# Performance work log

Measured on AMD Instinct MI355X. Metric: run time of the kernel, lower is better.

Reference implementation:

```python
import jax, jax.numpy as jnp
import numpy as np

N_EMBD = 1024
N_HEAD = 16
HEAD_DIM = N_EMBD // N_HEAD

def setup_inputs() -> dict:
    key = jax.random.key(0)
    ks = jax.random.split(key, 9)
    B, T, C = 2, 2048, N_EMBD
    s = 1.0 / np.sqrt(C)
    x = jax.random.normal(ks[0], (B, T, C), dtype=jnp.float32)
    Wk = jax.random.normal(ks[1], (C, C), dtype=jnp.float32) * s
    bk = jnp.zeros((C,), dtype=jnp.float32)
    Wq = jax.random.normal(ks[2], (C, C), dtype=jnp.float32) * s
    bq = jnp.zeros((C,), dtype=jnp.float32)
    Wv = jax.random.normal(ks[3], (C, C), dtype=jnp.float32) * s
    bv = jnp.zeros((C,), dtype=jnp.float32)
    Wp = jax.random.normal(ks[4], (C, C), dtype=jnp.float32) * s
    bp = jnp.zeros((C,), dtype=jnp.float32)
    return {"x": x, "Wq": Wq, "bq": bq, "Wk": Wk, "bk": bk, "Wv": Wv, "bv": bv, "Wp": Wp, "bp": bp}

def reference(x, Wq, bq, Wk, bk, Wv, bv, Wp, bp):
    B, T, C = x.shape
    H, D = N_HEAD, HEAD_DIM
    # QKV projections (torch Linear: x @ W.T + b; here W is stored as (in,out))
    q = (x @ Wq + bq).reshape(B, T, H, D).transpose(0, 2, 1, 3)  # [B,H,T,D]
    k = (x @ Wk + bk).reshape(B, T, H, D).transpose(0, 2, 1, 3)
    v = (x @ Wv + bv).reshape(B, T, H, D).transpose(0, 2, 1, 3)
    att = jnp.einsum('bhtd,bhsd->bhts', q, k) / jnp.sqrt(jnp.float32(D))
    causal = jnp.tril(jnp.ones((T, T), dtype=bool))
    att = jnp.where(causal, att, jnp.float32(-jnp.inf))
    att = jax.nn.softmax(att, axis=-1)
    y = jnp.einsum('bhts,bhsd->bhtd', att, v)  # [B,H,T,D]
    y = y.transpose(0, 2, 1, 3).reshape(B, T, C)
    return y @ Wp + bp
```

## Files before the change

### kernel.cpp

```cpp
#include <hip/hip_runtime.h>
#include <cstdint>

typedef __attribute__((ext_vector_type(4))) short s16x4;
typedef __attribute__((ext_vector_type(8))) short s16x8;
typedef __attribute__((ext_vector_type(4))) float f32x4;
typedef __attribute__((ext_vector_type(16))) float f32x16;

#define L2E 1.44269504088896340736f

__device__ __forceinline__ short f2bf(float f) {
  union { float f; unsigned u; } v; v.f = f;
  unsigned r = (v.u + 0x7fffu + ((v.u >> 16) & 1u)) >> 16;
  return (short)r;
}

__device__ __forceinline__ float xhalf_f(float x) {
  union { float f; unsigned u; } a; a.f = x;
  auto r = __builtin_amdgcn_permlane32_swap(a.u, a.u, false, false);
  union { unsigned u; float f; } b;
  b.u = (threadIdx.x & 32) ? r[0] : r[1];
  return b.f;
}

typedef const __attribute__((address_space(1))) unsigned int* gas_p;
typedef __attribute__((address_space(3))) unsigned int* las_p;
__device__ __forceinline__ void stage16(const void* g, void* l) {
  __builtin_amdgcn_global_load_lds((gas_p)(uintptr_t)g,
                                   (las_p)(unsigned int)(uintptr_t)l, 16, 0, 0);
}

__global__ __launch_bounds__(256) void prepass(const float* __restrict__ W0,
                                               const float* __restrict__ W1,
                                               const float* __restrict__ W2,
                                               const float* __restrict__ W3,
                                               short* __restrict__ wdst,
                                               const float* __restrict__ x,
                                               short* __restrict__ xb) {
  const int z = blockIdx.z;
  const int t = threadIdx.x;
  if (z >= 4) {
    int i = ((z - 4) * 256 + blockIdx.y * 16 + blockIdx.x) * 256 + t;
    const f32x4* p = (const f32x4*)x + (size_t)i * 2;
    f32x4 a = p[0], b = p[1];
    s16x8 o;
    o[0] = f2bf(a[0]); o[1] = f2bf(a[1]); o[2] = f2bf(a[2]); o[3] = f2bf(a[3]);
    o[4] = f2bf(b[0]); o[5] = f2bf(b[1]); o[6] = f2bf(b[2]); o[7] = f2bf(b[3]);
    *((s16x8*)xb + i) = o;
    return;
  }
  __shared__ float tile[64][65];
  const float* in = (z == 0) ? W0 : (z == 1) ? W1 : (z == 2) ? W2 : W3;
  short* out = wdst + (size_t)z * 1048576;
  const int bi = blockIdx.y, bj = blockIdx.x;
  const int c = t & 63, r0 = t >> 6;
#pragma unroll
  for (int i = 0; i < 16; i++) {
    int r = r0 + i * 4;
    tile[r][c] = in[(size_t)(bi * 64 + r) * 1024 + bj * 64 + c];
  }
  __syncthreads();
#pragma unroll
  for (int i = 0; i < 16; i++) {
    int r = r0 + i * 4;
    out[(size_t)(bj * 64 + r) * 1024 + bi * 64 + c] = f2bf(tile[c][r]);
  }
}

template <int EPI, int BM>
__global__ __launch_bounds__(BM * 2) void gemm_bt(
    const short* __restrict__ A, const short* __restrict__ B, int N, int K,
    const float* __restrict__ b0, const float* __restrict__ b1,
    const float* __restrict__ b2, short* __restrict__ o0, short* __restrict__ o1,
    short* __restrict__ o2, float* __restrict__ ofp) {
  constexpr int T = BM * 2;
  constexpr int AR = 2;
  constexpr int BR = 512 / T;
  constexpr int BUFB = (BM + 128) * 32;
  __shared__ short L[2 * BUFB];
  const int tid = threadIdx.x;
  const int lane = tid & 63;
  const int wave = tid >> 6;
  const int wr = wave >> 1, wc = wave & 1;
  const int l15 = lane & 15, l4 = lane >> 4;
  const int id = blockIdx.x + gridDim.x * blockIdx.y;
  const int cpx = gridDim.x >> 3;
  const int xcd = id & 7, sub = id >> 3;
  const int m0 = (sub / cpx) * BM;
  const int n0 = (xcd * cpx + sub % cpx) * 128;
  f32x4 acc[4][4];
#pragma unroll
  for (int i = 0; i < 4; i++)
#pragma unroll
    for (int j = 0; j < 4; j++) acc[i][j] = (f32x4){0.f, 0.f, 0.f, 0.f};

  const int lq = tid & 3, lr = tid >> 2;
  int soffA[AR], goffA[AR];
#pragma unroll
  for (int i = 0; i < AR; i++) {
    const int r = i * (T / 4) + lr;
    soffA[i] = r * 32 + lq * 8;
    goffA[i] = r * K + lq * 8;
  }
  int soffB[BR], goffB[BR];
#pragma unroll
  for (int j = 0; j < BR; j++) {
    const int r = j * (T / 4) + lr;
    soffB[j] = BM * 32 + r * 32 + lq * 8;
    goffB[j] = r * K + lq * 8;
  }

  const short* Asrc = A + (size_t)m0 * K;
  const short* Bsrc = B + (size_t)n0 * K;
  short* bufC = L;
  short* bufN = L + BUFB;

#define GSTAGE(BUF)                                                            \
  {                                                                            \
    _Pragma("unroll") for (int i_ = 0; i_ < AR; i_++)                          \
        stage16(Asrc + goffA[i_], (BUF) + soffA[i_]);                          \
    _Pragma("unroll") for (int j_ = 0; j_ < BR; j_++)                          \
        stage16(Bsrc + goffB[j_], (BUF) + soffB[j_]);                          \
    Asrc += 32; Bsrc += 32;                                                    \
  }

  GSTAGE(bufC)
  const int NK = K >> 5;
  for (int kt = 0; kt < NK; kt++) {
    __syncthreads();
    if (kt + 1 < NK) GSTAGE(bufN)
    s16x8 af[4], bfr[4];
#pragma unroll
    for (int i = 0; i < 4; i++) {
      af[i] = *(const s16x8*)(bufC + (wr * 64 + i * 16 + l15) * 32 + l4 * 8);
      bfr[i] = *(const s16x8*)(bufC + BM * 32 + (wc * 64 + i * 16 + l15) * 32 + l4 * 8);
    }
#pragma unroll
    for (int mi = 0; mi < 4; mi++)
#pragma unroll
      for (int ni = 0; ni < 4; ni++)
        acc[mi][ni] = __builtin_amdgcn_mfma_f32_16x16x32_bf16(af[mi], bfr[ni],
                                                              acc[mi][ni], 0, 0, 0);
    short* t_ = bufC; bufC = bufN; bufN = t_;
  }
#undef GSTAGE

#pragma unroll
  for (int ni = 0; ni < 4; ni++) {
    const int col = n0 + wc * 64 + ni * 16 + l15;
    if (EPI == 1) {
      const float bias = b0[col];
#pragma unroll
      for (int mi = 0; mi < 4; mi++)
#pragma unroll
        for (int r = 0; r < 4; r++) {
          int row = m0 + wr * 64 + mi * 16 + l4 * 4 + r;
          ofp[(size_t)row * N + col] = acc[mi][ni][r] + bias;
        }
    } else {
      const float* bp; short* dst; int c1; int isV = 0; float scl = 1.0f;
      if (col < 1024) { bp = b0; dst = o0; c1 = col; scl = 0.125f * L2E; }
      else if (col < 2048) { bp = b1; dst = o1; c1 = col - 1024; }
      else { bp = b2; dst = o2; c1 = col - 2048; isV = 1; }
      const float bias = bp[c1];
      const int h = c1 >> 6, d = c1 & 63;
      if (isV) {
#pragma unroll
        for (int mi = 0; mi < 4; mi++) {
          int t0 = m0 + wr * 64 + mi * 16 + l4 * 4;
          int bb = t0 >> 11, t = t0 & 2047;
          s16x4 ov;
#pragma unroll
          for (int r = 0; r < 4; r++) ov[r] = f2bf(acc[mi][ni][r] + bias);
          *(s16x4*)(dst + (size_t)((bb * 16 + h) * 64 + d) * 2048 + t) = ov;
        }
      } else {
#pragma unroll
        for (int mi = 0; mi < 4; mi++)
#pragma unroll
          for (int r = 0; r < 4; r++) {
            int row = m0 + wr * 64 + mi * 16 + l4 * 4 + r;
            int bb = row >> 11, t = row & 2047;
            float v = (acc[mi][ni][r] + bias) * scl;
            dst[(size_t)((bb * 16 + h) * 2048 + t) * 64 + d] = f2bf(v);
          }
      }
    }
  }
}

__global__ __launch_bounds__(128) void attn_v8(const short* __restrict__ Q,
                                               const short* __restrict__ K,
                                               const short* __restrict__ Vt,
                                               short* __restrict__ Y) {
  __shared__ short Ks[2][64 * 64];
  __shared__ short Vs[3][64 * 64];
  const int bh = blockIdx.x;
  const int y = blockIdx.y;
  const int g = y >> 3, r_ = y & 7;
  const int qbase = (g << 3) | ((g & 1) ? (7 - r_) : r_);
  const int qt = (qbase + ((bh & 3) << 3)) & 31;
  const int tid = threadIdx.x, lane = tid & 63, wave = tid >> 6;
  const int q31 = lane & 31, hi = lane >> 5;
  const short* Qp = Q + (size_t)bh * 2048 * 64;
  const short* Kp = K + (size_t)bh * 2048 * 64;
  const short* Vp = Vt + (size_t)bh * 64 * 2048;
  const int qrow = qt * 64 + wave * 32 + q31;
  const int nt = qt + 1;
  const int cx = q31 & 7;

  s16x8 qf[4];
#pragma unroll
  for (int s = 0; s < 4; s++)
    qf[s] = *(const s16x8*)(Qp + (size_t)qrow * 64 + s * 16 + hi * 8);

  f32x16 accA, accB, Z;
#pragma unroll
  for (int i = 0; i < 16; i++) { accA[i] = 0.f; accB[i] = 0.f; Z[i] = 0.f; }
  float l = 0.f;

  const int srow = tid >> 3, sch = tid & 7;
  int sdst[4], koff[4], voff[4];
#pragma unroll
  for (int i = 0; i < 4; i++) {
    const int r = srow + i * 16;
    const int sc = sch ^ (r & 7);
    sdst[i] = r * 64 + sch * 8;
    koff[i] = r * 64 + sc * 8;
    voff[i] = r * 2048 + sc * 8;
  }
  const short* kst = Kp;
  const short* vst = Vp;
  int rd0[4];
#pragma unroll
  for (int s = 0; s < 4; s++) rd0[s] = q31 * 64 + (((2 * s + hi) ^ cx) << 3);

  short* kA = &Ks[0][0]; short* kB = &Ks[1][0];
  short* vP = &Vs[2][0]; short* vC = &Vs[0][0]; short* vN = &Vs[1][0];

#pragma unroll
  for (int i = 0; i < 4; i++) {
    stage16(kst + koff[i], kA + sdst[i]);
    stage16(vst + voff[i], vC + sdst[i]);
  }
  kst += 4096; vst += 64;

#define STAGE_NEXT(COND)                                                       \
  if (COND) {                                                                  \
    _Pragma("unroll") for (int i_ = 0; i_ < 4; i_++) {                         \
      stage16(kst + koff[i_], kB + sdst[i_]);                                  \
      stage16(vst + voff[i_], vN + sdst[i_]);                                  \
    }                                                                          \
    kst += 4096; vst += 64;                                                    \
  }

#define QK(S0, S1)                                                             \
  {                                                                            \
    s16x8 kf0_[4], kf1_[4];                                                    \
    _Pragma("unroll") for (int s_ = 0; s_ < 4; s_++) {                         \
      kf0_[s_] = *(const s16x8*)(kA + rd0[s_]);                                \
      kf1_[s_] = *(const s16x8*)(kA + rd0[s_] + 2048);                         \
    }                                                                          \
    __builtin_amdgcn_s_setprio(1);                                             \
    S0 = __builtin_amdgcn_mfma_f32_32x32x16_bf16(kf0_[0], qf[0], Z, 0, 0, 0);  \
    S1 = __builtin_amdgcn_mfma_f32_32x32x16_bf16(kf1_[0], qf[0], Z, 0, 0, 0);  \
    _Pragma("unroll") for (int s_ = 1; s_ < 4; s_++) {                         \
      S0 = __builtin_amdgcn_mfma_f32_32x32x16_bf16(kf0_[s_], qf[s_], S0, 0, 0, 0); \
      S1 = __builtin_amdgcn_mfma_f32_32x32x16_bf16(kf1_[s_], qf[s_], S1, 0, 0, 0); \
    }                                                                          \
    __builtin_amdgcn_s_setprio(0);                                             \
  }

#define SMPV_BODY(S0, S1)                                                      \
  {                                                                            \
    float rsum_ = 0.f;                                                         \
    _Pragma("unroll") for (int r2_ = 0; r2_ < 16; r2_++) {                     \
      float p_ = __builtin_amdgcn_exp2f(S0[r2_]);                              \
      S0[r2_] = p_; rsum_ += p_;                                               \
    }                                                                          \
    _Pragma("unroll") for (int r2_ = 0; r2_ < 16; r2_++) {                     \
      float p_ = __builtin_amdgcn_exp2f(S1[r2_]);                              \
      S1[r2_] = p_; rsum_ += p_;                                               \
    }                                                                          \
    l += rsum_;                                                                \
    unsigned pk0_[8], pk1_[8];                                                 \
    _Pragma("unroll") for (int j_ = 0; j_ < 8; j_++) {                         \
      unsigned u_;                                                             \
      float a0_ = S0[2 * j_], a1_ = S0[2 * j_ + 1];                            \
      asm("v_cvt_pk_bf16_f32 %0, %1, %2" : "=v"(u_) : "v"(a0_), "v"(a1_));     \
      pk0_[j_] = u_;                                                           \
      float b0_ = S1[2 * j_], b1_ = S1[2 * j_ + 1];                            \
      asm("v_cvt_pk_bf16_f32 %0, %1, %2" : "=v"(u_) : "v"(b0_), "v"(b1_));     \
      pk1_[j_] = u_;                                                           \
    }                                                                          \
    _Pragma("unroll") for (int s_ = 0; s_ < 4; s_++) {                         \
      const unsigned* pk_ = (s_ < 2) ? pk0_ : pk1_;                            \
      const int b_ = 4 * (s_ & 1);                                             \
      auto rA_ = __builtin_amdgcn_permlane32_swap(pk_[b_ + 0], pk_[b_ + 2], false, false); \
      auto rB_ = __builtin_amdgcn_permlane32_swap(pk_[b_ + 1], pk_[b_ + 3], false, false); \
      union { unsigned u[4]; s16x8 v; } fr_;                                   \
      fr_.u[0] = rA_[0]; fr_.u[1] = rB_[0]; fr_.u[2] = rA_[1]; fr_.u[3] = rB_[1]; \
      s16x8 vf0_ = *(const s16x8*)(vP + rd0[s_]);                              \
      s16x8 vf1_ = *(const s16x8*)(vP + rd0[s_] + 2048);                       \
      __builtin_amdgcn_s_setprio(1);                                           \
      accA = __builtin_amdgcn_mfma_f32_32x32x16_bf16(vf0_, fr_.v, accA, 0, 0, 0); \
      accB = __builtin_amdgcn_mfma_f32_32x32x16_bf16(vf1_, fr_.v, accB, 0, 0, 0); \
      __builtin_amdgcn_s_setprio(0);                                           \
    }                                                                          \
  }

#define SMPV_MASK(S0, S1)                                                      \
  {                                                                            \
    const int k0_ = (nt - 1) * 64;                                             \
    _Pragma("unroll") for (int r2_ = 0; r2_ < 16; r2_++) {                     \
      int kvr_ = k0_ + (r2_ & 3) + 8 * (r2_ >> 2) + 4 * hi;                    \
      if (kvr_ > qrow) S0[r2_] = -__builtin_inff();                            \
      if (kvr_ + 32 > qrow) S1[r2_] = -__builtin_inff();                       \
    }                                                                          \
    SMPV_BODY(S0, S1)                                                          \
  }

#define ROT()                                                                  \
  {                                                                            \
    short* t_ = kA; kA = kB; kB = t_;                                          \
    t_ = vP; vP = vC; vC = vN; vN = t_;                                        \
  }

  f32x16 sA0, sA1, sB0, sB1;
  __syncthreads();
  STAGE_NEXT(nt > 1)
  QK(sA0, sA1)
  ROT()
  int t = 1;
  for (; t + 1 < nt; t += 2) {
    __syncthreads();
    STAGE_NEXT(t + 1 < nt)
    QK(sB0, sB1)
    SMPV_BODY(sA0, sA1)
    ROT()
    __syncthreads();
    STAGE_NEXT(t + 2 < nt)
    QK(sA0, sA1)
    SMPV_BODY(sB0, sB1)
    ROT()
  }
  if (t < nt) {
    __syncthreads();
    QK(sB0, sB1)
    SMPV_BODY(sA0, sA1)
    ROT()
    SMPV_MASK(sB0, sB1)
  } else {
    SMPV_MASK(sA0, sA1)
  }
#undef STAGE_NEXT
#undef QK
#undef SMPV_BODY
#undef SMPV_MASK
#undef ROT

  const int b_ = bh >> 4, h_ = bh & 15;
  const float lt = l + xhalf_f(l);
  const float invl = 1.f / lt;
  const size_t base = ((size_t)b_ * 2048 + qrow) * 1024 + h_ * 64;
#pragma unroll
  for (int gg = 0; gg < 4; gg++) {
    s16x4 o0, o1;
#pragma unroll
    for (int e = 0; e < 4; e++) {
      o0[e] = f2bf(accA[4 * gg + e] * invl);
      o1[e] = f2bf(accB[4 * gg + e] * invl);
    }
    *(s16x4*)(Y + base + 8 * gg + 4 * hi) = o0;
    *(s16x4*)(Y + base + 32 + 8 * gg + 4 * hi) = o1;
  }
}

extern "C" void kernel_launch(void* const* d_in, const int* in_sizes, int n_in,
                              void* d_out, int out_size, void* d_ws, size_t ws_size,
                              hipStream_t stream) {
  const float* x = (const float*)d_in[0];
  const float* Wq = (const float*)d_in[1];
  const float* bq = (const float*)d_in[2];
  const float* Wk = (const float*)d_in[3];
  const float* bk = (const float*)d_in[4];
  const float* Wv = (const float*)d_in[5];
  const float* bv = (const float*)d_in[6];
  const float* Wp = (const float*)d_in[7];
  const float* bp = (const float*)d_in[8];
  float* out = (float*)d_out;
  char* ws = (char*)d_ws;

  short* xb    = (short*)(ws + 0);
  short* WqkvT = (short*)(ws + 8388608);
  short* WpT   = (short*)(ws + 14680064);
  short* Qb    = (short*)(ws + 16777216);
  short* Kb    = (short*)(ws + 25165824);
  short* Vtb   = (short*)(ws + 33554432);
  short* Yb    = xb;

  prepass<<<dim3(16, 16, 12), 256, 0, stream>>>(Wq, Wk, Wv, Wp, WqkvT, x, xb);
  gemm_bt<0, 128><<<dim3(24, 32), 256, 0, stream>>>(xb, WqkvT, 3072, 1024, bq, bk,
                                                    bv, Qb, Kb, Vtb, nullptr);
  attn_v8<<<dim3(32, 32), 128, 0, stream>>>(Qb, Kb, Vtb, Yb);
  gemm_bt<1, 64><<<dim3(8, 64), 128, 0, stream>>>(Yb, WpT, 1024, 1024, bp, nullptr,
                                                  nullptr, nullptr, nullptr,
                                                  nullptr, out);
}
```

Baseline: 106.1 us.

## Replace QKV GEMM with 256x256-tile 8-wave kernel with interleaved staging

```diff
diff --git a/kernel.cpp b/kernel.cpp
--- a/kernel.cpp
+++ b/kernel.cpp
@@ -66,12 +66,158 @@
   }
 }
 
+__global__ __launch_bounds__(512) void gemm_qkv8(
+    const short* __restrict__ A, const short* __restrict__ B,
+    const float* __restrict__ b0, const float* __restrict__ b1,
+    const float* __restrict__ b2, short* __restrict__ o0,
+    short* __restrict__ o1, short* __restrict__ o2) {
+  constexpr int K = 1024, NKT = 16;
+  __shared__ short L[2 * 32768];
+  const int tid = threadIdx.x;
+  const int lane = tid & 63, wave = tid >> 6;
+  const int wr = wave >> 2, wc = wave & 3;
+  const int l15 = lane & 15, l4 = lane >> 4;
+  const int id = blockIdx.x;
+  const int wgid = (id & 7) * 24 + (id >> 3);
+  const int m0 = (wgid & 15) * 256;
+  const int n0 = (wgid >> 4) * 256;
+  const short* Asrc = A + (size_t)m0 * K;
+  const short* Bsrc = B + (size_t)n0 * K;
+
+  f32x4 acc[8][4];
+#pragma unroll
+  for (int i = 0; i < 8; i++)
+#pragma unroll
+    for (int j = 0; j < 4; j++) acc[i][j] = (f32x4){0.f, 0.f, 0.f, 0.f};
+
+  int sALo[2], gALo[2], sBLo[2], gBLo[2];
+#pragma unroll
+  for (int j = 0; j < 2; j++) {
+    const int flat = j * 512 + tid;
+    const int r = flat >> 3, ch = flat & 7;
+    const int sw8 = ((ch ^ (r & 7)) << 3);
+    sALo[j] = (r >> 6) * 8192 + (r & 63) * 64 + (ch << 3);
+    gALo[j] = ((r >> 6) * 128 + (r & 63)) * K + sw8;
+    sBLo[j] = 16384 + (flat << 3);
+    gBLo[j] = r * K + sw8;
+  }
+  int aoff[2], boff[2];
+#pragma unroll
+  for (int kf = 0; kf < 2; kf++) {
+    const int x = (((kf << 2) + l4) ^ (l15 & 7)) << 3;
+    aoff[kf] = wr * 8192 + l15 * 64 + x;
+    boff[kf] = 16384 + (wc >> 1) * 8192 + (wc & 1) * 4096 + l15 * 64 + x;
+  }
+
+#define ST_ALO(BB, T)                                                          \
+  { _Pragma("unroll") for (int j_ = 0; j_ < 2; j_++)                           \
+        stage16(Asrc + gALo[j_] + (T)*64, L + (BB) + sALo[j_]); }
+#define ST_AHI(BB, T)                                                          \
+  { _Pragma("unroll") for (int j_ = 0; j_ < 2; j_++)                           \
+        stage16(Asrc + gALo[j_] + 64 * K + (T)*64, L + (BB) + sALo[j_] + 4096); }
+#define ST_BLO(BB, T)                                                          \
+  { _Pragma("unroll") for (int j_ = 0; j_ < 2; j_++)                           \
+        stage16(Bsrc + gBLo[j_] + (T)*64, L + (BB) + sBLo[j_]); }
+#define ST_BHI(BB, T)                                                          \
+  { _Pragma("unroll") for (int j_ = 0; j_ < 2; j_++)                           \
+        stage16(Bsrc + gBLo[j_] + 128 * K + (T)*64, L + (BB) + sBLo[j_] + 8192); }
+
+#define RD_A(MI0)                                                              \
+  { _Pragma("unroll") for (int q_ = 0; q_ < 2; q_++)                           \
+        _Pragma("unroll") for (int kf_ = 0; kf_ < 2; kf_++)                    \
+            af[q_][kf_] = *(const s16x8*)(bc + aoff[kf_] + ((MI0) + q_) * 1024); }
+
+#define BAR_MFMA(MI0)                                                          \
+  __builtin_amdgcn_s_barrier();                                                \
+  asm volatile("s_waitcnt lgkmcnt(0)" ::: "memory");                           \
+  __builtin_amdgcn_sched_barrier(0);                                           \
+  __builtin_amdgcn_s_setprio(1);                                               \
+  _Pragma("unroll") for (int q_ = 0; q_ < 2; q_++)                             \
+      _Pragma("unroll") for (int ni_ = 0; ni_ < 4; ni_++)                      \
+          _Pragma("unroll") for (int kf_ = 0; kf_ < 2; kf_++)                  \
+              acc[(MI0) + q_][ni_] = __builtin_amdgcn_mfma_f32_16x16x32_bf16(  \
+                  af[q_][kf_], bf[ni_][kf_], acc[(MI0) + q_][ni_], 0, 0, 0);   \
+  __builtin_amdgcn_s_setprio(0);                                               \
+  __builtin_amdgcn_s_barrier();
+
+  ST_ALO(0, 0) ST_AHI(0, 0) ST_BLO(0, 0) ST_BHI(0, 0)
+  ST_BLO(32768, 1) ST_BHI(32768, 1) ST_ALO(32768, 1)
+  asm volatile("s_waitcnt vmcnt(6)" ::: "memory");
+  __builtin_amdgcn_s_barrier();
+
+  int bufc = 0;
+  for (int t = 0; t < NKT; ++t) {
+    const int bufn = bufc ^ 32768;
+    const short* bc = L + bufc;
+    s16x8 bf[4][2], af[2][2];
+#pragma unroll
+    for (int ni_ = 0; ni_ < 4; ni_++)
+#pragma unroll
+      for (int kf_ = 0; kf_ < 2; kf_++)
+        bf[ni_][kf_] = *(const s16x8*)(bc + boff[kf_] + ni_ * 1024);
+    RD_A(0)
+    if (t + 1 < NKT) ST_AHI(bufn, t + 1)
+    BAR_MFMA(0)
+    RD_A(2)
+    if (t + 2 < NKT) ST_BLO(bufc, t + 2)
+    BAR_MFMA(2)
+    RD_A(4)
+    if (t + 2 < NKT) ST_BHI(bufc, t + 2)
+    BAR_MFMA(4)
+    RD_A(6)
+    if (t + 2 < NKT) {
+      ST_ALO(bufc, t + 2)
+      asm volatile("s_waitcnt vmcnt(6)" ::: "memory");
+    } else {
+      asm volatile("s_waitcnt vmcnt(0)" ::: "memory");
+    }
+    BAR_MFMA(6)
+    bufc = bufn;
+  }
+#undef ST_ALO
+#undef ST_AHI
+#undef ST_BLO
+#undef ST_BHI
+#undef RD_A
+#undef BAR_MFMA
+
+#pragma unroll
+  for (int ni = 0; ni < 4; ni++) {
+    const int col = n0 + wc * 64 + ni * 16 + l15;
+    const float* bp; short* dst; int c1; int isV = 0; float scl = 1.0f;
+    if (col < 1024) { bp = b0; dst = o0; c1 = col; scl = 0.125f * L2E; }
+    else if (col < 2048) { bp = b1; dst = o1; c1 = col - 1024; }
+    else { bp = b2; dst = o2; c1 = col - 2048; isV = 1; }
+    const float bias = bp[c1];
+    const int h = c1 >> 6, d = c1 & 63;
+    if (isV) {
+#pragma unroll
+      for (int mi = 0; mi < 8; mi++) {
+        int t0 = m0 + wr * 128 + mi * 16 + l4 * 4;
+        int bb = t0 >> 11, tt = t0 & 2047;
+        s16x4 ov;
+#pragma unroll
+        for (int rr = 0; rr < 4; rr++) ov[rr] = f2bf(acc[mi][ni][rr] + bias);
+        *(s16x4*)(dst + (size_t)((bb * 16 + h) * 64 + d) * 2048 + tt) = ov;
+      }
+    } else {
+#pragma unroll
+      for (int mi = 0; mi < 8; mi++)
+#pragma unroll
+        for (int rr = 0; rr < 4; rr++) {
+          int row = m0 + wr * 128 + mi * 16 + l4 * 4 + rr;
+          int bb = row >> 11, tt = row & 2047;
+          float v = (acc[mi][ni][rr] + bias) * scl;
+          dst[(size_t)((bb * 16 + h) * 2048 + tt) * 64 + d] = f2bf(v);
+        }
+    }
+  }
+}
+
 template <int EPI, int BM>
 __global__ __launch_bounds__(BM * 2) void gemm_bt(
     const short* __restrict__ A, const short* __restrict__ B, int N, int K,
-    const float* __restrict__ b0, const float* __restrict__ b1,
-    const float* __restrict__ b2, short* __restrict__ o0, short* __restrict__ o1,
-    short* __restrict__ o2, float* __restrict__ ofp) {
+    const float* __restrict__ b0, float* __restrict__ ofp) {
   constexpr int T = BM * 2;
   constexpr int AR = 2;
   constexpr int BR = 512 / T;
@@ -147,44 +293,14 @@
 #pragma unroll
   for (int ni = 0; ni < 4; ni++) {
     const int col = n0 + wc * 64 + ni * 16 + l15;
-    if (EPI == 1) {
-      const float bias = b0[col];
-#pragma unroll
-      for (int mi = 0; mi < 4; mi++)
-#pragma unroll
-        for (int r = 0; r < 4; r++) {
-          int row = m0 + wr * 64 + mi * 16 + l4 * 4 + r;
-          ofp[(size_t)row * N + col] = acc[mi][ni][r] + bias;
-        }
-    } else {
-      const float* bp; short* dst; int c1; int isV = 0; float scl = 1.0f;
-      if (col < 1024) { bp = b0; dst = o0; c1 = col; scl = 0.125f * L2E; }
-      else if (col < 2048) { bp = b1; dst = o1; c1 = col - 1024; }
-      else { bp = b2; dst = o2; c1 = col - 2048; isV = 1; }
-      const float bias = bp[c1];
-      const int h = c1 >> 6, d = c1 & 63;
-      if (isV) {
-#pragma unroll
-        for (int mi = 0; mi < 4; mi++) {
-          int t0 = m0 + wr * 64 + mi * 16 + l4 * 4;
-          int bb = t0 >> 11, t = t0 & 2047;
-          s16x4 ov;
-#pragma unroll
-          for (int r = 0; r < 4; r++) ov[r] = f2bf(acc[mi][ni][r] + bias);
-          *(s16x4*)(dst + (size_t)((bb * 16 + h) * 64 + d) * 2048 + t) = ov;
-        }
-      } else {
-#pragma unroll
-        for (int mi = 0; mi < 4; mi++)
-#pragma unroll
-          for (int r = 0; r < 4; r++) {
-            int row = m0 + wr * 64 + mi * 16 + l4 * 4 + r;
-            int bb = row >> 11, t = row & 2047;
-            float v = (acc[mi][ni][r] + bias) * scl;
-            dst[(size_t)((bb * 16 + h) * 2048 + t) * 64 + d] = f2bf(v);
-          }
+    const float bias = b0[col];
+#pragma unroll
+    for (int mi = 0; mi < 4; mi++)
+#pragma unroll
+      for (int r = 0; r < 4; r++) {
+        int row = m0 + wr * 64 + mi * 16 + l4 * 4 + r;
+        ofp[(size_t)row * N + col] = acc[mi][ni][r] + bias;
       }
-    }
   }
 }
 
@@ -399,10 +515,7 @@
   short* Yb    = xb;
 
   prepass<<<dim3(16, 16, 12), 256, 0, stream>>>(Wq, Wk, Wv, Wp, WqkvT, x, xb);
-  gemm_bt<0, 128><<<dim3(24, 32), 256, 0, stream>>>(xb, WqkvT, 3072, 1024, bq, bk,
-                                                    bv, Qb, Kb, Vtb, nullptr);
+  gemm_qkv8<<<192, 512, 0, stream>>>(xb, WqkvT, bq, bk, bv, Qb, Kb, Vtb);
   attn_v8<<<dim3(32, 32), 128, 0, stream>>>(Qb, Kb, Vtb, Yb);
-  gemm_bt<1, 64><<<dim3(8, 64), 128, 0, stream>>>(Yb, WpT, 1024, 1024, bp, nullptr,
-                                                  nullptr, nullptr, nullptr,
-                                                  nullptr, out);
-}
+  gemm_bt<1, 64><<<dim3(8, 64), 128, 0, stream>>>(Yb, WpT, 1024, 1024, bp, out);
+}
```

Result: no change. 104.5 us, median of 2 (-1.5%).

## Load K fragments directly from global into registers, bypassing LDS

Applied to the files above, without the earlier changes.

```diff
diff --git a/kernel.cpp b/kernel.cpp
--- a/kernel.cpp
+++ b/kernel.cpp
@@ -188,11 +188,10 @@
   }
 }
 
-__global__ __launch_bounds__(128) void attn_v8(const short* __restrict__ Q,
+__global__ __launch_bounds__(128) void attn_v9(const short* __restrict__ Q,
                                                const short* __restrict__ K,
                                                const short* __restrict__ Vt,
                                                short* __restrict__ Y) {
-  __shared__ short Ks[2][64 * 64];
   __shared__ short Vs[3][64 * 64];
   const int bh = blockIdx.x;
   const int y = blockIdx.y;
@@ -219,69 +218,79 @@
   float l = 0.f;
 
   const int srow = tid >> 3, sch = tid & 7;
-  int sdst[4], koff[4], voff[4];
+  int sdst[4], voff[4];
 #pragma unroll
   for (int i = 0; i < 4; i++) {
     const int r = srow + i * 16;
     const int sc = sch ^ (r & 7);
     sdst[i] = r * 64 + sch * 8;
-    koff[i] = r * 64 + sc * 8;
     voff[i] = r * 2048 + sc * 8;
   }
-  const short* kst = Kp;
   const short* vst = Vp;
+  const short* kld = Kp;
   int rd0[4];
-#pragma unroll
-  for (int s = 0; s < 4; s++) rd0[s] = q31 * 64 + (((2 * s + hi) ^ cx) << 3);
-
-  short* kA = &Ks[0][0]; short* kB = &Ks[1][0];
+  int rdk[4];
+#pragma unroll
+  for (int s = 0; s < 4; s++) {
+    rd0[s] = q31 * 64 + (((2 * s + hi) ^ cx) << 3);
+    rdk[s] = q31 * 64 + ((2 * s + hi) << 3);
+  }
+
   short* vP = &Vs[2][0]; short* vC = &Vs[0][0]; short* vN = &Vs[1][0];
-
-#pragma unroll
-  for (int i = 0; i < 4; i++) {
-    stage16(kst + koff[i], kA + sdst[i]);
-    stage16(vst + voff[i], vC + sdst[i]);
-  }
-  kst += 4096; vst += 64;
-
-#define STAGE_NEXT(COND)                                                       \
+  s16x8 ka0[4], ka1[4], kb0[4], kb1[4];
+
+#pragma unroll
+  for (int i = 0; i < 4; i++) stage16(vst + voff[i], vC + sdst[i]);
+  vst += 64;
+#pragma unroll
+  for (int s = 0; s < 4; s++) {
+    ka0[s] = *(const s16x8*)(kld + rdk[s]);
+    ka1[s] = *(const s16x8*)(kld + rdk[s] + 2048);
+  }
+  kld += 4096;
+
+#define STAGE_NEXT(COND, KN0, KN1)                                             \
   if (COND) {                                                                  \
-    _Pragma("unroll") for (int i_ = 0; i_ < 4; i_++) {                         \
-      stage16(kst + koff[i_], kB + sdst[i_]);                                  \
-      stage16(vst + voff[i_], vN + sdst[i_]);                                  \
-    }                                                                          \
-    kst += 4096; vst += 64;                                                    \
-  }
-
-#define QK(S0, S1)                                                             \
+    _Pragma("unroll") for (int i_ = 0; i_ < 4; i_++)                           \
+        stage16(vst + voff[i_], vN + sdst[i_]);                                \
+    vst += 64;                                                                 \
+    _Pragma("unroll") for (int s_ = 0; s_ < 4; s_++) {                         \
+      KN0[s_] = *(const s16x8*)(kld + rdk[s_]);                                \
+      KN1[s_] = *(const s16x8*)(kld + rdk[s_] + 2048);                         \
+    }                                                                          \
+    kld += 4096;                                                               \
+  }
+
+#define QK_STEP(T, S0, S1, KC0, KC1, KN0, KN1)                                 \
   {                                                                            \
-    s16x8 kf0_[4], kf1_[4];                                                    \
-    _Pragma("unroll") for (int s_ = 0; s_ < 4; s_++) {                         \
-      kf0_[s_] = *(const s16x8*)(kA + rd0[s_]);                                \
-      kf1_[s_] = *(const s16x8*)(kA + rd0[s_] + 2048);                         \
-    }                                                                          \
+    __syncthreads();                                                           \
+    STAGE_NEXT((T) + 1 < nt, KN0, KN1)                                         \
     __builtin_amdgcn_s_setprio(1);                                             \
-    S0 = __builtin_amdgcn_mfma_f32_32x32x16_bf16(kf0_[0], qf[0], Z, 0, 0, 0);  \
-    S1 = __builtin_amdgcn_mfma_f32_32x32x16_bf16(kf1_[0], qf[0], Z, 0, 0, 0);  \
+    S0 = __builtin_amdgcn_mfma_f32_32x32x16_bf16(KC0[0], qf[0], Z, 0, 0, 0);   \
+    S1 = __builtin_amdgcn_mfma_f32_32x32x16_bf16(KC1[0], qf[0], Z, 0, 0, 0);   \
     _Pragma("unroll") for (int s_ = 1; s_ < 4; s_++) {                         \
-      S0 = __builtin_amdgcn_mfma_f32_32x32x16_bf16(kf0_[s_], qf[s_], S0, 0, 0, 0); \
-      S1 = __builtin_amdgcn_mfma_f32_32x32x16_bf16(kf1_[s_], qf[s_], S1, 0, 0, 0); \
+      S0 = __builtin_amdgcn_mfma_f32_32x32x16_bf16(KC0[s_], qf[s_], S0, 0, 0, 0); \
+      S1 = __builtin_amdgcn_mfma_f32_32x32x16_bf16(KC1[s_], qf[s_], S1, 0, 0, 0); \
     }                                                                          \
     __builtin_amdgcn_s_setprio(0);                                             \
   }
 
 #define SMPV_BODY(S0, S1)                                                      \
   {                                                                            \
-    float rsum_ = 0.f;                                                         \
+    float rs0_ = 0.f, rs1_ = 0.f, rs2_ = 0.f, rs3_ = 0.f;                      \
     _Pragma("unroll") for (int r2_ = 0; r2_ < 16; r2_++) {                     \
       float p_ = __builtin_amdgcn_exp2f(S0[r2_]);                              \
-      S0[r2_] = p_; rsum_ += p_;                                               \
+      S0[r2_] = p_;                                                            \
+      if ((r2_ & 3) == 0) rs0_ += p_; else if ((r2_ & 3) == 1) rs1_ += p_;     \
+      else if ((r2_ & 3) == 2) rs2_ += p_; else rs3_ += p_;                    \
     }                                                                          \
     _Pragma("unroll") for (int r2_ = 0; r2_ < 16; r2_++) {                     \
       float p_ = __builtin_amdgcn_exp2f(S1[r2_]);                              \
-      S1[r2_] = p_; rsum_ += p_;                                               \
-    }                                                                          \
-    l += rsum_;                                                                \
+      S1[r2_] = p_;                                                            \
+      if ((r2_ & 3) == 0) rs0_ += p_; else if ((r2_ & 3) == 1) rs1_ += p_;     \
+      else if ((r2_ & 3) == 2) rs2_ += p_; else rs3_ += p_;                    \
+    }                                                                          \
+    l += (rs0_ + rs1_) + (rs2_ + rs3_);                                        \
     unsigned pk0_[8], pk1_[8];                                                 \
     _Pragma("unroll") for (int j_ = 0; j_ < 8; j_++) {                         \
       unsigned u_;                                                             \
@@ -320,32 +329,22 @@
   }
 
 #define ROT()                                                                  \
-  {                                                                            \
-    short* t_ = kA; kA = kB; kB = t_;                                          \
-    t_ = vP; vP = vC; vC = vN; vN = t_;                                        \
-  }
+  { short* t_ = vP; vP = vC; vC = vN; vN = t_; }
 
   f32x16 sA0, sA1, sB0, sB1;
-  __syncthreads();
-  STAGE_NEXT(nt > 1)
-  QK(sA0, sA1)
+  QK_STEP(0, sA0, sA1, ka0, ka1, kb0, kb1)
   ROT()
   int t = 1;
   for (; t + 1 < nt; t += 2) {
-    __syncthreads();
-    STAGE_NEXT(t + 1 < nt)
-    QK(sB0, sB1)
+    QK_STEP(t, sB0, sB1, kb0, kb1, ka0, ka1)
     SMPV_BODY(sA0, sA1)
     ROT()
-    __syncthreads();
-    STAGE_NEXT(t + 2 < nt)
-    QK(sA0, sA1)
+    QK_STEP(t + 1, sA0, sA1, ka0, ka1, kb0, kb1)
     SMPV_BODY(sB0, sB1)
     ROT()
   }
   if (t < nt) {
-    __syncthreads();
-    QK(sB0, sB1)
+    QK_STEP(t, sB0, sB1, kb0, kb1, ka0, ka1)
     SMPV_BODY(sA0, sA1)
     ROT()
     SMPV_MASK(sB0, sB1)
@@ -353,7 +352,7 @@
     SMPV_MASK(sA0, sA1)
   }
 #undef STAGE_NEXT
-#undef QK
+#undef QK_STEP
 #undef SMPV_BODY
 #undef SMPV_MASK
 #undef ROT
@@ -401,7 +400,7 @@
   prepass<<<dim3(16, 16, 12), 256, 0, stream>>>(Wq, Wk, Wv, Wp, WqkvT, x, xb);
   gemm_bt<0, 128><<<dim3(24, 32), 256, 0, stream>>>(xb, WqkvT, 3072, 1024, bq, bk,
                                                     bv, Qb, Kb, Vtb, nullptr);
-  attn_v8<<<dim3(32, 32), 128, 0, stream>>>(Qb, Kb, Vtb, Yb);
+  attn_v9<<<dim3(32, 32), 128, 0, stream>>>(Qb, Kb, Vtb, Yb);
   gemm_bt<1, 64><<<dim3(8, 64), 128, 0, stream>>>(Yb, WpT, 1024, 1024, bp, nullptr,
                                                   nullptr, nullptr, nullptr,
                                                   nullptr, out);
```

New measurement: 122.1 us. 1.15x slower.

## Widen attention blocks to 128 query rows with four waves sharing K/V tiles

Applied to the files above, without the earlier changes.

```diff
diff --git a/kernel.cpp b/kernel.cpp
--- a/kernel.cpp
+++ b/kernel.cpp
@@ -188,24 +188,24 @@
   }
 }
 
-__global__ __launch_bounds__(128) void attn_v8(const short* __restrict__ Q,
-                                               const short* __restrict__ K,
-                                               const short* __restrict__ Vt,
-                                               short* __restrict__ Y) {
+__global__ __launch_bounds__(256) void attn_v10(const short* __restrict__ Q,
+                                                const short* __restrict__ K,
+                                                const short* __restrict__ Vt,
+                                                short* __restrict__ Y) {
   __shared__ short Ks[2][64 * 64];
   __shared__ short Vs[3][64 * 64];
   const int bh = blockIdx.x;
   const int y = blockIdx.y;
-  const int g = y >> 3, r_ = y & 7;
-  const int qbase = (g << 3) | ((g & 1) ? (7 - r_) : r_);
-  const int qt = (qbase + ((bh & 3) << 3)) & 31;
+  const int q0 = (y & 8) ? (y & 7) : (15 - (y & 7));
+  const int qt = (bh & 1) ? (15 - q0) : q0;
   const int tid = threadIdx.x, lane = tid & 63, wave = tid >> 6;
   const int q31 = lane & 31, hi = lane >> 5;
   const short* Qp = Q + (size_t)bh * 2048 * 64;
   const short* Kp = K + (size_t)bh * 2048 * 64;
   const short* Vp = Vt + (size_t)bh * 64 * 2048;
-  const int qrow = qt * 64 + wave * 32 + q31;
-  const int nt = qt + 1;
+  const int qrow = qt * 128 + wave * 32 + q31;
+  const int nt = 2 * qt + 2;
+  const int ntw = 2 * qt + 1 + (wave >> 1);
   const int cx = q31 & 7;
 
   s16x8 qf[4];
@@ -219,10 +219,10 @@
   float l = 0.f;
 
   const int srow = tid >> 3, sch = tid & 7;
-  int sdst[4], koff[4], voff[4];
-#pragma unroll
-  for (int i = 0; i < 4; i++) {
-    const int r = srow + i * 16;
+  int sdst[2], koff[2], voff[2];
+#pragma unroll
+  for (int i = 0; i < 2; i++) {
+    const int r = srow + i * 32;
     const int sc = sch ^ (r & 7);
     sdst[i] = r * 64 + sch * 8;
     koff[i] = r * 64 + sc * 8;
@@ -238,7 +238,7 @@
   short* vP = &Vs[2][0]; short* vC = &Vs[0][0]; short* vN = &Vs[1][0];
 
 #pragma unroll
-  for (int i = 0; i < 4; i++) {
+  for (int i = 0; i < 2; i++) {
     stage16(kst + koff[i], kA + sdst[i]);
     stage16(vst + voff[i], vC + sdst[i]);
   }
@@ -246,42 +246,58 @@
 
 #define STAGE_NEXT(COND)                                                       \
   if (COND) {                                                                  \
-    _Pragma("unroll") for (int i_ = 0; i_ < 4; i_++) {                         \
+    _Pragma("unroll") for (int i_ = 0; i_ < 2; i_++) {                         \
       stage16(kst + koff[i_], kB + sdst[i_]);                                  \
       stage16(vst + voff[i_], vN + sdst[i_]);                                  \
     }                                                                          \
     kst += 4096; vst += 64;                                                    \
   }
 
-#define QK(S0, S1)                                                             \
+#define QK_STEP(T, S0, S1)                                                     \
   {                                                                            \
-    s16x8 kf0_[4], kf1_[4];                                                    \
-    _Pragma("unroll") for (int s_ = 0; s_ < 4; s_++) {                         \
-      kf0_[s_] = *(const s16x8*)(kA + rd0[s_]);                                \
-      kf1_[s_] = *(const s16x8*)(kA + rd0[s_] + 2048);                         \
-    }                                                                          \
-    __builtin_amdgcn_s_setprio(1);                                             \
-    S0 = __builtin_amdgcn_mfma_f32_32x32x16_bf16(kf0_[0], qf[0], Z, 0, 0, 0);  \
-    S1 = __builtin_amdgcn_mfma_f32_32x32x16_bf16(kf1_[0], qf[0], Z, 0, 0, 0);  \
-    _Pragma("unroll") for (int s_ = 1; s_ < 4; s_++) {                         \
-      S0 = __builtin_amdgcn_mfma_f32_32x32x16_bf16(kf0_[s_], qf[s_], S0, 0, 0, 0); \
-      S1 = __builtin_amdgcn_mfma_f32_32x32x16_bf16(kf1_[s_], qf[s_], S1, 0, 0, 0); \
-    }                                                                          \
-    __builtin_amdgcn_s_setprio(0);                                             \
-  }
-
-#define SMPV_BODY(S0, S1)                                                      \
-  {                                                                            \
-    float rsum_ = 0.f;                                                         \
+    __syncthreads();                                                           \
+    STAGE_NEXT((T) + 1 < nt)                                                   \
+    if ((T) < ntw) {                                                           \
+      s16x8 kf0_[4], kf1_[4];                                                  \
+      _Pragma("unroll") for (int s_ = 0; s_ < 4; s_++) {                       \
+        kf0_[s_] = *(const s16x8*)(kA + rd0[s_]);                              \
+        kf1_[s_] = *(const s16x8*)(kA + rd0[s_] + 2048);                       \
+      }                                                                        \
+      __builtin_amdgcn_s_setprio(1);                                           \
+      S0 = __builtin_amdgcn_mfma_f32_32x32x16_bf16(kf0_[0], qf[0], Z, 0, 0, 0);\
+      S1 = __builtin_amdgcn_mfma_f32_32x32x16_bf16(kf1_[0], qf[0], Z, 0, 0, 0);\
+      _Pragma("unroll") for (int s_ = 1; s_ < 4; s_++) {                       \
+        S0 = __builtin_amdgcn_mfma_f32_32x32x16_bf16(kf0_[s_], qf[s_], S0, 0, 0, 0); \
+        S1 = __builtin_amdgcn_mfma_f32_32x32x16_bf16(kf1_[s_], qf[s_], S1, 0, 0, 0); \
+      }                                                                        \
+      __builtin_amdgcn_s_setprio(0);                                           \
+    }                                                                          \
+  }
+
+#define SMPV(T, S0, S1)                                                        \
+  if ((T) < ntw) {                                                             \
+    if ((T) == ntw - 1) {                                                      \
+      const int k0_ = (T)*64;                                                  \
+      _Pragma("unroll") for (int r2_ = 0; r2_ < 16; r2_++) {                   \
+        int kvr_ = k0_ + (r2_ & 3) + 8 * (r2_ >> 2) + 4 * hi;                  \
+        if (kvr_ > qrow) S0[r2_] = -__builtin_inff();                          \
+        if (kvr_ + 32 > qrow) S1[r2_] = -__builtin_inff();                     \
+      }                                                                        \
+    }                                                                          \
+    float rs0_ = 0.f, rs1_ = 0.f, rs2_ = 0.f, rs3_ = 0.f;                      \
     _Pragma("unroll") for (int r2_ = 0; r2_ < 16; r2_++) {                     \
       float p_ = __builtin_amdgcn_exp2f(S0[r2_]);                              \
-      S0[r2_] = p_; rsum_ += p_;                                               \
+      S0[r2_] = p_;                                                            \
+      if ((r2_ & 3) == 0) rs0_ += p_; else if ((r2_ & 3) == 1) rs1_ += p_;     \
+      else if ((r2_ & 3) == 2) rs2_ += p_; else rs3_ += p_;                    \
     }                                                                          \
     _Pragma("unroll") for (int r2_ = 0; r2_ < 16; r2_++) {                     \
       float p_ = __builtin_amdgcn_exp2f(S1[r2_]);                              \
-      S1[r2_] = p_; rsum_ += p_;                                               \
-    }                                                                          \
-    l += rsum_;                                                                \
+      S1[r2_] = p_;                                                            \
+      if ((r2_ & 3) == 0) rs0_ += p_; else if ((r2_ & 3) == 1) rs1_ += p_;     \
+      else if ((r2_ & 3) == 2) rs2_ += p_; else rs3_ += p_;                    \
+    }                                                                          \
+    l += (rs0_ + rs1_) + (rs2_ + rs3_);                                        \
     unsigned pk0_[8], pk1_[8];                                                 \
     _Pragma("unroll") for (int j_ = 0; j_ < 8; j_++) {                         \
       unsigned u_;                                                             \
@@ -308,17 +324,6 @@
     }                                                                          \
   }
 
-#define SMPV_MASK(S0, S1)                                                      \
-  {                                                                            \
-    const int k0_ = (nt - 1) * 64;                                             \
-    _Pragma("unroll") for (int r2_ = 0; r2_ < 16; r2_++) {                     \
-      int kvr_ = k0_ + (r2_ & 3) + 8 * (r2_ >> 2) + 4 * hi;                    \
-      if (kvr_ > qrow) S0[r2_] = -__builtin_inff();                            \
-      if (kvr_ + 32 > qrow) S1[r2_] = -__builtin_inff();                       \
-    }                                                                          \
-    SMPV_BODY(S0, S1)                                                          \
-  }
-
 #define ROT()                                                                  \
   {                                                                            \
     short* t_ = kA; kA = kB; kB = t_;                                          \
@@ -326,36 +331,24 @@
   }
 
   f32x16 sA0, sA1, sB0, sB1;
-  __syncthreads();
-  STAGE_NEXT(nt > 1)
-  QK(sA0, sA1)
+  QK_STEP(0, sA0, sA1)
   ROT()
   int t = 1;
   for (; t + 1 < nt; t += 2) {
-    __syncthreads();
-    STAGE_NEXT(t + 1 < nt)
-    QK(sB0, sB1)
-    SMPV_BODY(sA0, sA1)
+    QK_STEP(t, sB0, sB1)
+    SMPV(t - 1, sA0, sA1)
     ROT()
-    __syncthreads();
-    STAGE_NEXT(t + 2 < nt)
-    QK(sA0, sA1)
-    SMPV_BODY(sB0, sB1)
+    QK_STEP(t + 1, sA0, sA1)
+    SMPV(t, sB0, sB1)
     ROT()
   }
-  if (t < nt) {
-    __syncthreads();
-    QK(sB0, sB1)
-    SMPV_BODY(sA0, sA1)
-    ROT()
-    SMPV_MASK(sB0, sB1)
-  } else {
-    SMPV_MASK(sA0, sA1)
-  }
+  QK_STEP(nt - 1, sB0, sB1)
+  SMPV(nt - 2, sA0, sA1)
+  ROT()
+  SMPV(nt - 1, sB0, sB1)
 #undef STAGE_NEXT
-#undef QK
-#undef SMPV_BODY
-#undef SMPV_MASK
+#undef QK_STEP
+#undef SMPV
 #undef ROT
 
   const int b_ = bh >> 4, h_ = bh & 15;
@@ -401,7 +394,7 @@
   prepass<<<dim3(16, 16, 12), 256, 0, stream>>>(Wq, Wk, Wv, Wp, WqkvT, x, xb);
   gemm_bt<0, 128><<<dim3(24, 32), 256, 0, stream>>>(xb, WqkvT, 3072, 1024, bq, bk,
                                                     bv, Qb, Kb, Vtb, nullptr);
-  attn_v8<<<dim3(32, 32), 128, 0, stream>>>(Qb, Kb, Vtb, Yb);
+  attn_v10<<<dim3(32, 16), 256, 0, stream>>>(Qb, Kb, Vtb, Yb);
   gemm_bt<1, 64><<<dim3(8, 64), 128, 0, stream>>>(Yb, WpT, 1024, 1024, bp, nullptr,
                                                   nullptr, nullptr, nullptr,
                                                   nullptr, out);
```

Result: no change. 106.7 us (+0.5%).
